# Kernel tuning notes

Hardware: AMD Instinct MI355X
Metric: run time of the kernel (lower is better)

Reference implementation:

```python
import jax, jax.numpy as jnp
import numpy as np

WIDE = 15
PAD = (WIDE - 1) // 2
FREQS = np.array([1., 2., 3., 4., 5., 6.], dtype=np.float32)  # wave_base_ml frequencies


def _lstm_dir(x, wih, whh, b):
    # x: [B,T,F]; wih: [4H,F]; whh: [4H,H]; b: [4H] (b_ih+b_hh fused)
    H = whh.shape[1]
    xg = jnp.einsum('btf,gf->btg', x, wih) + b  # precompute input projections
    def step(carry, xt):
        h, c = carry
        g = xt + h @ whh.T
        i, f, gg, o = jnp.split(g, 4, axis=-1)  # torch gate order i,f,g,o
        c = jax.nn.sigmoid(f) * c + jax.nn.sigmoid(i) * jnp.tanh(gg)
        h = jax.nn.sigmoid(o) * jnp.tanh(c)
        return (h, c), h
    h0 = jnp.zeros((x.shape[0], H), x.dtype)
    _, hs = jax.lax.scan(step, (h0, h0), jnp.swapaxes(xg, 0, 1))
    return jnp.swapaxes(hs, 0, 1)


def _bn(x, g, b, eps=1e-5):
    # training-mode BatchNorm1d over (N, L) per channel; x: [B,C,L]
    m = jnp.mean(x, axis=(0, 2), keepdims=True)
    v = jnp.var(x, axis=(0, 2), keepdims=True)
    return (x - m) * jax.lax.rsqrt(v + eps) * g[None, :, None] + b[None, :, None]


def _conv1d(x, w, b):
    y = jax.lax.conv_general_dilated(x, w, (1,), 'VALID', dimension_numbers=('NCH', 'OIH', 'NCH'))
    return y + b[None, :, None]


def _haar(x):
    s = 0.7071067811865476
    return (x[..., ::2] + x[..., 1::2]) * s, (x[..., ::2] - x[..., 1::2]) * s


def _forward(x, lstm_wif, lstm_whf, lstm_bf, lstm_wir, lstm_whr, lstm_br, base_w, base_b,
             g1, be1, g2, be2, g3, be3, g4, be4, g5, be5,
             w2, b2, w3, b3, w4, b4, w5, b5, fcw, fcb):
    xt = jnp.swapaxes(x, 1, 2)  # [B,T,F]
    fwd = _lstm_dir(xt, lstm_wif, lstm_whf, lstm_bf)
    bwd = _lstm_dir(xt[:, ::-1], lstm_wir, lstm_whr, lstm_br)[:, ::-1]
    X = jnp.swapaxes(jnp.concatenate([fwd, bwd], axis=-1), 1, 2)  # [B,C,T], C=2*dim
    B, C, T = X.shape
    Xp = jnp.pad(X, ((0, 0), (0, 0), (PAD, PAD)))
    # shared sliding windows [B,C,T,WIDE] used both for scale conv and Furi_conv
    Xwin = jnp.stack([Xp[..., k:k + T] for k in range(WIDE)], axis=-1)
    offs = (jnp.arange(WIDE, dtype=X.dtype) - PAD) / WIDE
    outs = []
    for ii in range(len(FREQS)):
        scales = jax.nn.relu(jnp.einsum('bctk,k->bct', Xwin, base_w[ii]) + base_b[ii])
        # per-position cosine Fourier basis generated from the learned scales
        bases = jnp.cos((2.0 * np.pi * FREQS[ii]) * scales[..., None] * offs)  # [B,C,T,WIDE]
        o = jnp.sum(Xwin * bases, axis=-1)  # position-dependent (dynamic) conv
        sqrs = jnp.sqrt((jnp.trunc(scales * WIDE) + 1.0) / (WIDE + 2) * 2.0)
        outs.append(o / sqrs)
    wave = jnp.stack(outs, axis=1).reshape(B, -1, T)  # [B, n_waves*C, T] (wave-major, matches torch cat+view)
    out = _bn(wave, g1, be1)
    out = _bn(jax.nn.relu(_conv1d(out, w2, b2)), g2, be2)
    out = _bn(jax.nn.relu(_conv1d(out, w3, b3)), g3, be3)
    out_back = out  # [B, V_dim, L3]
    out = _bn(jax.nn.relu(_conv1d(out, w4, b4)), g4, be4)  # [B,16,L3-2]
    # 4-level Haar DWT; 5 subbands upsampled to L3, averaged over channels
    a1, d1 = _haar(out_back); a2, d2 = _haar(a1); a3, d3 = _haar(a2); a4, d4 = _haar(a3)
    L3 = out_back.shape[-1]
    bands = [jnp.repeat(bb, L3 // bb.shape[-1], axis=-1) for bb in (a4, d4, d3, d2, d1)]
    dwt = jnp.stack([bb.mean(axis=1) for bb in bands], axis=1)  # [B,5,L3]
    odwt = _bn(jax.nn.relu(_conv1d(dwt, w5, b5)), g5, be5)  # [B,16,L3-2]
    out = jnp.concatenate([out, odwt], axis=-1)
    out = out.mean(axis=-1)  # AdaptiveAvgPool1d(1) + squeeze
    return out @ fcw.T + fcb


def setup_inputs() -> dict:
    key = jax.random.key(0)
    ks = iter(jax.random.split(key, 40))
    def p(shape, s=0.05):
        return jax.random.normal(next(ks), shape, jnp.float32) * s
    B, F, T, DIM, NW, Vd = 32, 64, 518, 64, 6, 32
    C = 2 * DIM
    return {
        'x': jax.random.normal(next(ks), (B, F, T), jnp.float32),
        'lstm_wif': p((4 * DIM, F)), 'lstm_whf': p((4 * DIM, DIM)), 'lstm_bf': p((4 * DIM,)),
        'lstm_wir': p((4 * DIM, F)), 'lstm_whr': p((4 * DIM, DIM)), 'lstm_br': p((4 * DIM,)),
        'base_w': p((NW, WIDE)), 'base_b': p((NW,)),
        'g1': jnp.ones((C * NW,)), 'be1': jnp.zeros((C * NW,)),
        'g2': jnp.ones((128,)), 'be2': jnp.zeros((128,)),
        'g3': jnp.ones((Vd,)), 'be3': jnp.zeros((Vd,)),
        'g4': jnp.ones((16,)), 'be4': jnp.zeros((16,)),
        'g5': jnp.ones((16,)), 'be5': jnp.zeros((16,)),
        'w2': p((128, C * NW, 3)), 'b2': p((128,)),
        'w3': p((Vd, 128, 5)), 'b3': p((Vd,)),
        'w4': p((16, Vd, 3)), 'b4': p((16,)),
        'w5': p((16, 5, 3)), 'b5': p((16,)),
        'fcw': p((10, 16)), 'fcb': p((10,)),
    }


def reference(x, lstm_wif, lstm_whf, lstm_bf, lstm_wir, lstm_whr, lstm_br, base_w, base_b,
              g1, be1, g2, be2, g3, be3, g4, be4, g5, be5,
              w2, b2, w3, b3, w4, b4, w5, b5, fcw, fcb):
    return _forward(x, lstm_wif, lstm_whf, lstm_bf, lstm_wir, lstm_whr, lstm_br, base_w, base_b,
                    g1, be1, g2, be2, g3, be3, g4, be4, g5, be5,
                    w2, b2, w3, b3, w4, b4, w5, b5, fcw, fcb)
```

## Files before the change

### kernel.cpp

```cpp
#include <hip/hip_runtime.h>
#include <math.h>

#define B_     32
#define F_     64
#define T_     518
#define HID    64
#define GATES  256
#define CCH    128
#define NWAVE  6
#define WCH    768
#define L2_    516
#define L3_    512
#define L4_    510

typedef float v2f __attribute__((ext_vector_type(2)));
typedef _Float16 h2 __attribute__((ext_vector_type(2)));

__device__ __forceinline__ float frcp(float x) { return __builtin_amdgcn_rcpf(x); }
__device__ __forceinline__ float fsigmoid(float x) { return frcp(1.f + __expf(-x)); }
__device__ __forceinline__ float ftanh(float x) { return 1.f - 2.f * frcp(1.f + __expf(2.f * x)); }

__device__ __forceinline__ float fdot2(h2 a, h2 b, float c) {
#if __has_builtin(__builtin_amdgcn_fdot2)
    return __builtin_amdgcn_fdot2(a, b, c, false);
#else
    return fmaf((float)a[0], (float)b[0], fmaf((float)a[1], (float)b[1], c));
#endif
}

__global__ void packw_kernel(const float* __restrict__ whf, const float* __restrict__ whr,
                             h2* __restrict__ w16f, h2* __restrict__ w16r) {
    const int row = threadIdx.x;
    const float* sf = whf + (size_t)row * HID;
    const float* sr = whr + (size_t)row * HID;
#pragma unroll
    for (int i = 0; i < 32; ++i) {
        w16f[row * 32 + i] = (h2){(_Float16)sf[2 * i], (_Float16)sf[2 * i + 1]};
        w16r[row * 32 + i] = (h2){(_Float16)sr[2 * i], (_Float16)sr[2 * i + 1]};
    }
}

__global__ void xg_kernel(const float* __restrict__ x,
                          const float* __restrict__ wif, const float* __restrict__ bf,
                          const float* __restrict__ wir, const float* __restrict__ br,
                          float* __restrict__ xg_f, float* __restrict__ xg_r,
                          float* __restrict__ stats, float* __restrict__ stats23) {
    if (blockIdx.x == 0 && blockIdx.y == 0) {
        for (int i = threadIdx.x; i < 2 * WCH; i += 256) stats[i] = 0.f;
        if (threadIdx.x < 320) stats23[threadIdx.x] = 0.f;
    }
    const int tid = threadIdx.x;
    const int wv  = tid >> 7;
    const int g2  = tid & 1;
    const int r   = (tid >> 1) & 63;
    const int g   = (2 * wv + g2) * 64 + r;
    const int b   = blockIdx.y;
    const int t0  = blockIdx.x * 8;
    float4 wa[16], wb[16];
    const float4* w0 = (const float4*)(wif + g * F_);
    const float4* w1 = (const float4*)(wir + g * F_);
#pragma unroll
    for (int i = 0; i < 16; ++i) { wa[i] = w0[i]; wb[i] = w1[i]; }
    const float bfv = bf[g], brv = br[g];
    for (int tt = 0; tt < 8; ++tt) {
        const int t = t0 + tt;
        if (t >= T_) break;
        const float* xp = x + (size_t)b * F_ * T_ + t;
        float a0 = bfv, a1 = brv;
#pragma unroll
        for (int i = 0; i < 16; ++i) {
            float x0 = xp[(i * 4 + 0) * T_];
            float x1 = xp[(i * 4 + 1) * T_];
            float x2 = xp[(i * 4 + 2) * T_];
            float x3 = xp[(i * 4 + 3) * T_];
            a0 += wa[i].x * x0 + wa[i].y * x1 + wa[i].z * x2 + wa[i].w * x3;
            a1 += wb[i].x * x0 + wb[i].y * x1 + wb[i].z * x2 + wb[i].w * x3;
        }
        const size_t o = ((size_t)b * T_ + t) * GATES + tid;
        xg_f[o] = a0;
        xg_r[o] = a1;
    }
}

__global__ __launch_bounds__(128, 1) void lstm_kernel(
        const float* __restrict__ xgi_f, const float* __restrict__ xgi_r,
        const h2* __restrict__ w16f, const h2* __restrict__ w16r,
        float* __restrict__ X) {
    const int dir = blockIdx.x & 1;
    const int b   = blockIdx.x >> 1;
    const float* xg  = (dir ? xgi_r : xgi_f) + (size_t)b * T_ * GATES;
    const h2* w16 = dir ? w16r : w16f;
    const int tid = threadIdx.x;
    const int r   = tid & 63;
    const int w   = tid >> 6;

    union U4 { uint4 u; h2 h[4]; };
    U4 wA[8], wB[8];
    {
        const uint4* pA = (const uint4*)(w16 + (size_t)((2 * w) * HID + r) * 32);
        const uint4* pB = (const uint4*)(w16 + (size_t)((2 * w + 1) * HID + r) * 32);
#pragma unroll
        for (int i = 0; i < 8; ++i) { wA[i].u = pA[i]; wB[i].u = pB[i]; }
    }

    __shared__ __align__(16) _Float16 hs16[2][HID];
    __shared__ __align__(16) float gbuf[2][HID][4];
    hs16[w][r] = (_Float16)0.f;
    float c = 0.f;
    float* Xrow = X + ((size_t)(b * CCH + dir * HID + r)) * T_;

    int t = dir ? (T_ - 1) : 0;
    const int step = dir ? -1 : 1;
    const float2* xg2 = (const float2*)xg;
    float2 q0 = xg2[((size_t)t * 2 + w) * 64 + r];
    float2 q1 = xg2[((size_t)(t + step) * 2 + w) * 64 + r];

    for (int s = 0; s < T_; ++s) {
        float a0 = q0.x, a0b = 0.f;
        float a1 = q0.y, a1b = 0.f;
        const uint4* hp4 = (const uint4*)hs16[w];
#pragma unroll
        for (int i = 0; i < 8; ++i) {
            U4 hv; hv.u = hp4[i];
            a0  = fdot2(wA[i].h[0], hv.h[0], a0);
            a0b = fdot2(wA[i].h[1], hv.h[1], a0b);
            a0  = fdot2(wA[i].h[2], hv.h[2], a0);
            a0b = fdot2(wA[i].h[3], hv.h[3], a0b);
            a1  = fdot2(wB[i].h[0], hv.h[0], a1);
            a1b = fdot2(wB[i].h[1], hv.h[1], a1b);
            a1  = fdot2(wB[i].h[2], hv.h[2], a1);
            a1b = fdot2(wB[i].h[3], hv.h[3], a1b);
        }
        const float gA = a0 + a0b;
        const float gB = a1 + a1b;
        const int buf = s & 1;
        *(float2*)&gbuf[buf][r][2 * w] = make_float2(gA, gB);

        int tp = t + 2 * step;
        tp = tp < 0 ? 0 : (tp >= T_ ? T_ - 1 : tp);
        const float2 qn = xg2[((size_t)tp * 2 + w) * 64 + r];

        asm volatile("s_waitcnt lgkmcnt(0)" ::: "memory");
        __builtin_amdgcn_s_barrier();

        const float4 g4 = *(const float4*)gbuf[buf][r];
        const float si = fsigmoid(g4.x);
        const float sf = fsigmoid(g4.y);
        const float so = fsigmoid(g4.w);
        c = sf * c + si * ftanh(g4.z);
        const float h = so * ftanh(c);

        hs16[w][r] = (_Float16)h;
        if (w == 0) Xrow[t] = h;
        q0 = q1; q1 = qn;
        t += step;
    }
}

__global__ void wave_kernel(const float* __restrict__ X,
                            const float* __restrict__ bw, const float* __restrict__ bb,
                            float* __restrict__ wave, float* __restrict__ stats) {
    const int b = blockIdx.z, c = blockIdx.y;
    const int t0 = blockIdx.x * 256;
    const int tid = threadIdx.x;
    __shared__ float xs[256 + 14];
    __shared__ float bws[NWAVE][16];
    __shared__ float bbs[NWAVE];
    __shared__ float red[4][12];
    const float* xrow = X + ((size_t)(b * CCH + c)) * T_;
    for (int i = tid; i < 270; i += 256) {
        int tt = t0 - 7 + i;
        xs[i] = (tt >= 0 && tt < T_) ? xrow[tt] : 0.f;
    }
    if (tid < NWAVE * 15) bws[tid / 15][tid % 15] = bw[tid];
    if (tid < NWAVE) bbs[tid] = bb[tid];
    __syncthreads();
    const int t = t0 + tid;
    float ls[NWAVE], lq[NWAVE];
#pragma unroll
    for (int ii = 0; ii < NWAVE; ++ii) { ls[ii] = 0.f; lq[ii] = 0.f; }
    if (t < T_) {
        float win[15];
#pragma unroll
        for (int k = 0; k < 15; ++k) win[k] = xs[tid + k];
        float e[8];
        e[0] = win[7];
#pragma unroll
        for (int m = 1; m < 8; ++m) e[m] = win[7 - m] + win[7 + m];
        const float c0 = 6.28318530717958647692f / 15.f;
#pragma unroll
        for (int ii = 0; ii < NWAVE; ++ii) {
            float sc = bbs[ii];
#pragma unroll
            for (int k = 0; k < 15; ++k) sc += win[k] * bws[ii][k];
            sc = fmaxf(sc, 0.f);
            const float phi = c0 * (float)(ii + 1) * sc;
            float o = e[0];
#pragma unroll
            for (int m = 1; m < 8; ++m) o += e[m] * __cosf(phi * (float)m);
            const float q = (truncf(sc * 15.f) + 1.f) * (2.f / 17.f);
            const float val = o * rsqrtf(q);
            wave[((size_t)(b * WCH + ii * CCH + c)) * T_ + t] = val;
            ls[ii] = val;
            lq[ii] = val * val;
        }
    }
#pragma unroll
    for (int off = 32; off > 0; off >>= 1) {
#pragma unroll
        for (int ii = 0; ii < NWAVE; ++ii) {
            ls[ii] += __shfl_down(ls[ii], off);
            lq[ii] += __shfl_down(lq[ii], off);
        }
    }
    if ((tid & 63) == 0) {
        const int w = tid >> 6;
#pragma unroll
        for (int ii = 0; ii < NWAVE; ++ii) { red[w][ii] = ls[ii]; red[w][6 + ii] = lq[ii]; }
    }
    __syncthreads();
    if (tid < 12) {
        const float a = red[0][tid] + red[1][tid] + red[2][tid] + red[3][tid];
        const int ii = tid % 6;
        const int ch = ii * CCH + c;
        atomicAdd(&stats[(tid >= 6 ? WCH : 0) + ch], a);
    }
}

__global__ void bn1_finalize_kernel(const float* __restrict__ stats,
                                    float* __restrict__ mean, float* __restrict__ rstd) {
    const int c = threadIdx.x;
    const float n = (float)(B_ * T_);
    const float m = stats[c] / n;
    const float v = stats[WCH + c] / n - m * m;
    mean[c] = m;
    rstd[c] = rsqrtf(v + 1e-5f);
}

__global__ void bnfold2_kernel(const float* __restrict__ w2, const float* __restrict__ b2,
                               const float* __restrict__ m1, const float* __restrict__ r1,
                               const float* __restrict__ g1, const float* __restrict__ be1,
                               float* __restrict__ w2t, float* __restrict__ b2t) {
    const int o = blockIdx.x, tid = threadIdx.x;
    float part = 0.f;
    for (int idx = tid; idx < WCH * 3; idx += 256) {
        const int c = idx / 3;
        const float sc = r1[c] * g1[c];
        const float sh = be1[c] - m1[c] * sc;
        const float wv = w2[(size_t)o * (WCH * 3) + idx];
        w2t[(size_t)idx * 128 + o] = wv * sc;
        part += wv * sh;
    }
#pragma unroll
    for (int off = 32; off > 0; off >>= 1) part += __shfl_down(part, off);
    __shared__ float red[4];
    if ((tid & 63) == 0) red[tid >> 6] = part;
    __syncthreads();
    if (tid == 0) b2t[o] = b2[o] + red[0] + red[1] + red[2] + red[3];
}

__global__ void bnfold3_kernel(const float* __restrict__ w3, const float* __restrict__ b3,
                               const float* __restrict__ stats2,
                               const float* __restrict__ g2, const float* __restrict__ be2,
                               float* __restrict__ w3t, float* __restrict__ b3t) {
    const int o = blockIdx.x, tid = threadIdx.x;
    __shared__ float sc2s[128], sh2s[128];
    if (tid < 128) {
        const float n = (float)(B_ * L2_);
        const float m = stats2[tid] / n;
        const float v = stats2[128 + tid] / n - m * m;
        const float sc = rsqrtf(v + 1e-5f) * g2[tid];
        sc2s[tid] = sc;
        sh2s[tid] = be2[tid] - m * sc;
    }
    __syncthreads();
    float part = 0.f;
    for (int idx = tid; idx < 128 * 5; idx += 256) {
        const int c = idx / 5;
        const float wv = w3[(size_t)o * 640 + idx];
        w3t[(size_t)idx * 32 + o] = wv * sc2s[c];
        part += wv * sh2s[c];
    }
#pragma unroll
    for (int off = 32; off > 0; off >>= 1) part += __shfl_down(part, off);
    __shared__ float red[4];
    if ((tid & 63) == 0) red[tid >> 6] = part;
    __syncthreads();
    if (tid == 0) b3t[o] = b3[o] + red[0] + red[1] + red[2] + red[3];
}

__global__ void bnfold4_kernel(const float* __restrict__ w4, const float* __restrict__ b4,
                               const float* __restrict__ stats3,
                               const float* __restrict__ g3, const float* __restrict__ be3,
                               float* __restrict__ w4t, float* __restrict__ b4t) {
    const int o = blockIdx.x, tid = threadIdx.x;
    __shared__ float sc3s[32], sh3s[32];
    if (tid < 32) {
        const float n = (float)(B_ * L3_);
        const float m = stats3[tid] / n;
        const float v = stats3[32 + tid] / n - m * m;
        const float sc = rsqrtf(v + 1e-5f) * g3[tid];
        sc3s[tid] = sc;
        sh3s[tid] = be3[tid] - m * sc;
    }
    __syncthreads();
    float part = 0.f;
    if (tid < 96) {
        const int c = tid / 3;
        const float wv = w4[(size_t)o * 96 + tid];
        w4t[(size_t)tid * 16 + o] = wv * sc3s[c];
        part = wv * sh3s[c];
    }
#pragma unroll
    for (int off = 32; off > 0; off >>= 1) part += __shfl_down(part, off);
    __shared__ float red[2];
    if ((tid & 63) == 0) red[tid >> 6] = part;
    __syncthreads();
    if (tid == 0) b4t[o] = b4[o] + red[0] + red[1];
}

__global__ __launch_bounds__(256) void conv2_kernel(
        const float* __restrict__ in, const float* __restrict__ wt,
        const float* __restrict__ bt, float* __restrict__ out,
        float* __restrict__ stats2) {
    const int b  = blockIdx.x;
    const int tid = threadIdx.x;
    const int t  = blockIdx.y * 256 + tid;
    const int o0 = blockIdx.z * 16;
    float rv[16], qv[16];
#pragma unroll
    for (int j = 0; j < 16; ++j) rv[j] = 0.f;
    if (t < L2_) {
        v2f acc[8];
        const v2f* bt2 = (const v2f*)(bt + o0);
#pragma unroll
        for (int j = 0; j < 8; ++j) acc[j] = bt2[j];
        const float* inb = in + (size_t)b * WCH * T_ + t;
        for (int c = 0; c < WCH; ++c) {
            const float x0 = inb[c * T_], x1 = inb[c * T_ + 1], x2 = inb[c * T_ + 2];
            const v2f vx0 = {x0, x0}, vx1 = {x1, x1}, vx2 = {x2, x2};
            const v2f* wc = (const v2f*)(wt + (size_t)c * 384 + o0);
#pragma unroll
            for (int j = 0; j < 8; ++j)
                acc[j] = __builtin_elementwise_fma(wc[j], vx0,
                         __builtin_elementwise_fma(wc[64 + j], vx1,
                         __builtin_elementwise_fma(wc[128 + j], vx2, acc[j])));
        }
        const size_t ob = ((size_t)b * 128 + o0) * L2_ + t;
#pragma unroll
        for (int j = 0; j < 8; ++j) {
            rv[2 * j]     = fmaxf(acc[j].x, 0.f);
            rv[2 * j + 1] = fmaxf(acc[j].y, 0.f);
            out[ob + (size_t)(2 * j) * L2_]     = rv[2 * j];
            out[ob + (size_t)(2 * j + 1) * L2_] = rv[2 * j + 1];
        }
    }
#pragma unroll
    for (int j = 0; j < 16; ++j) qv[j] = rv[j] * rv[j];
#pragma unroll
    for (int off = 32; off > 0; off >>= 1) {
#pragma unroll
        for (int j = 0; j < 16; ++j) {
            rv[j] += __shfl_down(rv[j], off);
            qv[j] += __shfl_down(qv[j], off);
        }
    }
    __shared__ float red2[4][32];
    if ((tid & 63) == 0) {
        const int wv = tid >> 6;
#pragma unroll
        for (int j = 0; j < 16; ++j) { red2[wv][j] = rv[j]; red2[wv][16 + j] = qv[j]; }
    }
    __syncthreads();
    if (tid < 32) {
        const float a = red2[0][tid] + red2[1][tid] + red2[2][tid] + red2[3][tid];
        atomicAdd(&stats2[(tid >= 16 ? 128 : 0) + o0 + (tid & 15)], a);
    }
}

__global__ __launch_bounds__(256) void conv3_kernel(
        const float* __restrict__ in, const float* __restrict__ wt,
        const float* __restrict__ bt, float* __restrict__ out,
        float* __restrict__ stats3) {
    const int b  = blockIdx.x;
    const int tid = threadIdx.x;
    const int t  = blockIdx.y * 256 + tid;
    const int o0 = blockIdx.z * 8;
    v2f acc[4];
    const v2f* bt2 = (const v2f*)(bt + o0);
#pragma unroll
    for (int j = 0; j < 4; ++j) acc[j] = bt2[j];
    const float* inb = in + (size_t)b * 128 * L2_ + t;
    for (int c = 0; c < 128; ++c) {
        const float x0 = inb[c * L2_], x1 = inb[c * L2_ + 1], x2 = inb[c * L2_ + 2];
        const float x3 = inb[c * L2_ + 3], x4 = inb[c * L2_ + 4];
        const v2f vx0 = {x0, x0}, vx1 = {x1, x1}, vx2 = {x2, x2}, vx3 = {x3, x3}, vx4 = {x4, x4};
        const v2f* wc = (const v2f*)(wt + (size_t)c * 160 + o0);
#pragma unroll
        for (int j = 0; j < 4; ++j)
            acc[j] = __builtin_elementwise_fma(wc[j], vx0,
                     __builtin_elementwise_fma(wc[16 + j], vx1,
                     __builtin_elementwise_fma(wc[32 + j], vx2,
                     __builtin_elementwise_fma(wc[48 + j], vx3,
                     __builtin_elementwise_fma(wc[64 + j], vx4, acc[j])))));
    }
    const size_t ob = ((size_t)b * 32 + o0) * L3_ + t;
    float rv[8], qv[8];
#pragma unroll
    for (int j = 0; j < 4; ++j) {
        rv[2 * j]     = fmaxf(acc[j].x, 0.f);
        rv[2 * j + 1] = fmaxf(acc[j].y, 0.f);
        out[ob + (size_t)(2 * j) * L3_]     = rv[2 * j];
        out[ob + (size_t)(2 * j + 1) * L3_] = rv[2 * j + 1];
    }
#pragma unroll
    for (int j = 0; j < 8; ++j) qv[j] = rv[j] * rv[j];
#pragma unroll
    for (int off = 32; off > 0; off >>= 1) {
#pragma unroll
        for (int j = 0; j < 8; ++j) {
            rv[j] += __shfl_down(rv[j], off);
            qv[j] += __shfl_down(qv[j], off);
        }
    }
    __shared__ float red3[4][16];
    if ((tid & 63) == 0) {
        const int wv = tid >> 6;
#pragma unroll
        for (int j = 0; j < 8; ++j) { red3[wv][j] = rv[j]; red3[wv][8 + j] = qv[j]; }
    }
    __syncthreads();
    if (tid < 16) {
        const float a = red3[0][tid] + red3[1][tid] + red3[2][tid] + red3[3][tid];
        atomicAdd(&stats3[(tid >= 8 ? 32 : 0) + o0 + (tid & 7)], a);
    }
}

__global__ __launch_bounds__(512) void tail_fused_kernel(
        const float* __restrict__ y3, const float* __restrict__ w4t,
        const float* __restrict__ b4t, const float* __restrict__ w5,
        const float* __restrict__ b5, const float* __restrict__ stats3,
        const float* __restrict__ g3, const float* __restrict__ be3,
        float* __restrict__ part) {
    const int b = blockIdx.x, l = threadIdx.x;
    __shared__ float cm[L3_];
    __shared__ float bands[5][L3_];
    __shared__ float w5s[240];
    __shared__ float b5s[16], b4s[16];
    __shared__ float sc3s[32], sh3s[32];
    __shared__ float redf[8][64];
    if (l < 240) w5s[l] = w5[l];
    if (l < 16) { b5s[l] = b5[l]; b4s[l] = b4t[l]; }
    if (l >= 256 && l < 288) {
        const int ch = l - 256;
        const float n = (float)(B_ * L3_);
        const float m = stats3[ch] / n;
        const float v = stats3[32 + ch] / n - m * m;
        const float sc = rsqrtf(v + 1e-5f) * g3[ch];
        sc3s[ch] = sc;
        sh3s[ch] = be3[ch] - m * sc;
    }
    __syncthreads();
    v2f a4[8];
    const v2f* b4s2 = (const v2f*)b4s;
#pragma unroll
    for (int j = 0; j < 8; ++j) a4[j] = (v2f){0.f, 0.f};
    const float* yb = y3 + (size_t)b * 32 * L3_ + l;
    if (l < L4_) {
#pragma unroll
        for (int j = 0; j < 8; ++j) a4[j] = b4s2[j];
        for (int c = 0; c < 32; ++c) {
            const float x0 = yb[c * L3_], x1 = yb[c * L3_ + 1], x2 = yb[c * L3_ + 2];
            const v2f vx0 = {x0, x0}, vx1 = {x1, x1}, vx2 = {x2, x2};
            const v2f* wc = (const v2f*)(w4t + (size_t)c * 48);
#pragma unroll
            for (int j = 0; j < 8; ++j)
                a4[j] = __builtin_elementwise_fma(wc[j], vx0,
                        __builtin_elementwise_fma(wc[8 + j], vx1,
                        __builtin_elementwise_fma(wc[16 + j], vx2, a4[j])));
        }
    }
    {
        float s = 0.f, shs = 0.f;
        for (int ch = 0; ch < 32; ++ch) {
            s = fmaf(yb[ch * L3_], sc3s[ch], s);
            shs += sh3s[ch];
        }
        cm[l] = (s + shs) * (1.f / 32.f);
    }
    __syncthreads();
    const float s1 = 0.70710678118654752440f;
    const float s2c = 0.5f;
    const float s3 = 0.35355339059327378f;
    const float s4 = 0.25f;
    const int b16 = l & ~15, b8 = l & ~7, b4v = l & ~3, b2v = l & ~1;
    float sa = 0.f, sb = 0.f;
#pragma unroll
    for (int i = 0; i < 8; ++i) { sa += cm[b16 + i]; sb += cm[b16 + 8 + i]; }
    bands[0][l] = (sa + sb) * s4;
    bands[1][l] = (sa - sb) * s4;
    float ta = 0.f, tb = 0.f;
#pragma unroll
    for (int i = 0; i < 4; ++i) { ta += cm[b8 + i]; tb += cm[b8 + 4 + i]; }
    bands[2][l] = (ta - tb) * s3;
    bands[3][l] = (cm[b4v] + cm[b4v + 1] - cm[b4v + 2] - cm[b4v + 3]) * s2c;
    bands[4][l] = (cm[b2v] - cm[b2v + 1]) * s1;
    __syncthreads();
    float s4v[16], q4v[16], s5v[16], q5v[16];
#pragma unroll
    for (int o = 0; o < 16; ++o) { s5v[o] = 0.f; }
    if (l < L4_) {
        float in3[5][3];
#pragma unroll
        for (int c = 0; c < 5; ++c) {
            in3[c][0] = bands[c][l]; in3[c][1] = bands[c][l + 1]; in3[c][2] = bands[c][l + 2];
        }
#pragma unroll
        for (int o = 0; o < 16; ++o) {
            float acc = b5s[o];
#pragma unroll
            for (int c = 0; c < 5; ++c) {
                const float* wp = &w5s[(o * 5 + c) * 3];
                acc += in3[c][0] * wp[0] + in3[c][1] * wp[1] + in3[c][2] * wp[2];
            }
            s5v[o] = fmaxf(acc, 0.f);
        }
    }
#pragma unroll
    for (int j = 0; j < 8; ++j) {
        const float v0 = (l < L4_) ? fmaxf(a4[j].x, 0.f) : 0.f;
        const float v1 = (l < L4_) ? fmaxf(a4[j].y, 0.f) : 0.f;
        s4v[2 * j] = v0; s4v[2 * j + 1] = v1;
        q4v[2 * j] = v0 * v0; q4v[2 * j + 1] = v1 * v1;
    }
#pragma unroll
    for (int o = 0; o < 16; ++o) q5v[o] = s5v[o] * s5v[o];
#pragma unroll
    for (int off = 32; off > 0; off >>= 1) {
#pragma unroll
        for (int o = 0; o < 16; ++o) {
            s4v[o] += __shfl_down(s4v[o], off);
            q4v[o] += __shfl_down(q4v[o], off);
            s5v[o] += __shfl_down(s5v[o], off);
            q5v[o] += __shfl_down(q5v[o], off);
        }
    }
    if ((l & 63) == 0) {
        const int wv = l >> 6;
#pragma unroll
        for (int o = 0; o < 16; ++o) {
            redf[wv][o]      = s4v[o];
            redf[wv][16 + o] = q4v[o];
            redf[wv][32 + o] = s5v[o];
            redf[wv][48 + o] = q5v[o];
        }
    }
    __syncthreads();
    if (l < 64) {
        float a = 0.f;
#pragma unroll
        for (int wv = 0; wv < 8; ++wv) a += redf[wv][l];
        part[(size_t)(b * 16 + (l & 15)) * 4 + (l >> 4)] = a;
    }
}

__global__ __launch_bounds__(512) void tail_final_kernel(
        const float* __restrict__ part,
        const float* __restrict__ g4, const float* __restrict__ be4,
        const float* __restrict__ g5, const float* __restrict__ be5,
        const float* __restrict__ fcw, const float* __restrict__ fcb,
        float* __restrict__ out) {
    const int p = threadIdx.x;
    const int b = p >> 4, ch = p & 15;
    const float4 v = ((const float4*)part)[b * 16 + ch];
    __shared__ float S4[512], Q4[512], S5[512], Q5[512];
    __shared__ float M4[16], R4[16], M5[16], R5[16];
    __shared__ float pool[B_][16];
    S4[p] = v.x; Q4[p] = v.y; S5[p] = v.z; Q5[p] = v.w;
    __syncthreads();
    if (p < 16) {
        float ts = 0.f, tq = 0.f, us = 0.f, uq = 0.f;
        for (int bb = 0; bb < B_; ++bb) {
            ts += S4[bb * 16 + p]; tq += Q4[bb * 16 + p];
            us += S5[bb * 16 + p]; uq += Q5[bb * 16 + p];
        }
        const float n = (float)(B_ * L4_);
        float m = ts / n; M4[p] = m; R4[p] = rsqrtf(tq / n - m * m + 1e-5f);
        m = us / n;       M5[p] = m; R5[p] = rsqrtf(uq / n - m * m + 1e-5f);
    }
    __syncthreads();
    {
        const float mm4 = v.x / (float)L4_, mm5 = v.z / (float)L4_;
        const float v4 = (mm4 - M4[ch]) * R4[ch] * g4[ch] + be4[ch];
        const float v5 = (mm5 - M5[ch]) * R5[ch] * g5[ch] + be5[ch];
        pool[b][ch] = 0.5f * (v4 + v5);
    }
    __syncthreads();
    if (p < B_ * 10) {
        const int bb = p / 10, row = p - bb * 10;
        float a = fcb[row];
#pragma unroll
        for (int c = 0; c < 16; ++c) a += pool[bb][c] * fcw[row * 16 + c];
        out[bb * 10 + row] = a;
    }
}

extern "C" void kernel_launch(void* const* d_in, const int* in_sizes, int n_in,
                              void* d_out, int out_size, void* d_ws, size_t ws_size,
                              hipStream_t stream) {
    (void)in_sizes; (void)n_in; (void)out_size; (void)ws_size;
    const float* x   = (const float*)d_in[0];
    const float* wif = (const float*)d_in[1];
    const float* whf = (const float*)d_in[2];
    const float* bf  = (const float*)d_in[3];
    const float* wir = (const float*)d_in[4];
    const float* whr = (const float*)d_in[5];
    const float* br  = (const float*)d_in[6];
    const float* bw  = (const float*)d_in[7];
    const float* bb  = (const float*)d_in[8];
    const float* g1  = (const float*)d_in[9];  const float* be1 = (const float*)d_in[10];
    const float* g2  = (const float*)d_in[11]; const float* be2 = (const float*)d_in[12];
    const float* g3  = (const float*)d_in[13]; const float* be3 = (const float*)d_in[14];
    const float* g4  = (const float*)d_in[15]; const float* be4 = (const float*)d_in[16];
    const float* g5  = (const float*)d_in[17]; const float* be5 = (const float*)d_in[18];
    const float* w2  = (const float*)d_in[19]; const float* b2  = (const float*)d_in[20];
    const float* w3  = (const float*)d_in[21]; const float* b3  = (const float*)d_in[22];
    const float* w4  = (const float*)d_in[23]; const float* b4  = (const float*)d_in[24];
    const float* w5  = (const float*)d_in[25]; const float* b5  = (const float*)d_in[26];
    const float* fcw = (const float*)d_in[27]; const float* fcb = (const float*)d_in[28];
    float* out = (float*)d_out;
    float* ws  = (float*)d_ws;

    float* xg_f  = ws;
    float* xg_r  = ws + 4243456;
    float* wave  = ws;
    float* X     = ws + 12730368;
    float* y2    = ws + 14852096;
    float* y3    = ws + 16965632;
    float* stats = ws + 18012160;
    float* m1 = ws + 18013696; float* r1 = m1 + 768;
    float* tpart  = r1 + 768;
    float* stats2 = tpart + 2048;
    float* stats3 = stats2 + 256;
    float* w2t  = X;
    float* b2t  = X + 294912;
    float* w3t  = X + 295040;
    float* b3t  = X + 315520;
    float* w4t  = X + 315552;
    float* b4t  = X + 317088;
    h2* w16f = (h2*)y2;
    h2* w16r = (h2*)(y2 + 8192);

    packw_kernel<<<dim3(1), 256, 0, stream>>>(whf, whr, w16f, w16r);
    xg_kernel<<<dim3(65, 32), 256, 0, stream>>>(x, wif, bf, wir, br, xg_f, xg_r,
                                                stats, stats2);
    lstm_kernel<<<dim3(64), 128, 0, stream>>>(xg_f, xg_r, w16f, w16r, X);
    wave_kernel<<<dim3(3, CCH, B_), 256, 0, stream>>>(X, bw, bb, wave, stats);
    bn1_finalize_kernel<<<dim3(1), 768, 0, stream>>>(stats, m1, r1);
    bnfold2_kernel<<<dim3(128), 256, 0, stream>>>(w2, b2, m1, r1, g1, be1, w2t, b2t);
    conv2_kernel<<<dim3(32, 3, 8), 256, 0, stream>>>(wave, w2t, b2t, y2, stats2);
    bnfold3_kernel<<<dim3(32), 256, 0, stream>>>(w3, b3, stats2, g2, be2, w3t, b3t);
    conv3_kernel<<<dim3(32, 2, 4), 256, 0, stream>>>(y2, w3t, b3t, y3, stats3);
    bnfold4_kernel<<<dim3(16), 128, 0, stream>>>(w4, b4, stats3, g3, be3, w4t, b4t);
    tail_fused_kernel<<<dim3(B_), 512, 0, stream>>>(y3, w4t, b4t, w5, b5,
                                                    stats3, g3, be3, tpart);
    tail_final_kernel<<<dim3(1), 512, 0, stream>>>(tpart, g4, be4, g5, be5, fcw, fcb, out);
}
```

Measured before the change: 881.5 us.

## Remove LSTM gate LDS exchange, split xg by direction, use cosine recurrence, widen conv2

The LSTM step now pairs gate halves across wave lanes with shfl_xor instead of staging them in shared memory, and double-buffers the hidden state so each step needs one barrier instead of a store/barrier/load round trip. The input-projection kernel launches a third grid dimension for direction, halving per-thread weight registers. The wave kernel computes cos(m*phi) with a Chebyshev recurrence instead of seven cosf calls, and conv2 computes 32 output channels per block instead of 16. Together these target the serial LSTM latency and the ALU cost elsewhere, at the price of more registers in conv2 and possible small numeric drift from the recurrence.

```diff
diff --git a/kernel.cpp b/kernel.cpp
--- a/kernel.cpp
+++ b/kernel.cpp
@@ -45,10 +45,14 @@
                           const float* __restrict__ wir, const float* __restrict__ br,
                           float* __restrict__ xg_f, float* __restrict__ xg_r,
                           float* __restrict__ stats, float* __restrict__ stats23) {
-    if (blockIdx.x == 0 && blockIdx.y == 0) {
+    if (blockIdx.x == 0 && blockIdx.y == 0 && blockIdx.z == 0) {
         for (int i = threadIdx.x; i < 2 * WCH; i += 256) stats[i] = 0.f;
         if (threadIdx.x < 320) stats23[threadIdx.x] = 0.f;
     }
+    const int dir = blockIdx.z;
+    const float* wi = dir ? wir : wif;
+    const float* bi = dir ? br : bf;
+    float* xgo = dir ? xg_r : xg_f;
     const int tid = threadIdx.x;
     const int wv  = tid >> 7;
     const int g2  = tid & 1;
@@ -56,17 +60,16 @@
     const int g   = (2 * wv + g2) * 64 + r;
     const int b   = blockIdx.y;
     const int t0  = blockIdx.x * 8;
-    float4 wa[16], wb[16];
-    const float4* w0 = (const float4*)(wif + g * F_);
-    const float4* w1 = (const float4*)(wir + g * F_);
-#pragma unroll
-    for (int i = 0; i < 16; ++i) { wa[i] = w0[i]; wb[i] = w1[i]; }
-    const float bfv = bf[g], brv = br[g];
+    float4 wa[16];
+    const float4* w0 = (const float4*)(wi + g * F_);
+#pragma unroll
+    for (int i = 0; i < 16; ++i) wa[i] = w0[i];
+    const float bv = bi[g];
     for (int tt = 0; tt < 8; ++tt) {
         const int t = t0 + tt;
         if (t >= T_) break;
         const float* xp = x + (size_t)b * F_ * T_ + t;
-        float a0 = bfv, a1 = brv;
+        float a0 = bv;
 #pragma unroll
         for (int i = 0; i < 16; ++i) {
             float x0 = xp[(i * 4 + 0) * T_];
@@ -74,11 +77,8 @@
             float x2 = xp[(i * 4 + 2) * T_];
             float x3 = xp[(i * 4 + 3) * T_];
             a0 += wa[i].x * x0 + wa[i].y * x1 + wa[i].z * x2 + wa[i].w * x3;
-            a1 += wb[i].x * x0 + wb[i].y * x1 + wb[i].z * x2 + wb[i].w * x3;
-        }
-        const size_t o = ((size_t)b * T_ + t) * GATES + tid;
-        xg_f[o] = a0;
-        xg_r[o] = a1;
+        }
+        xgo[((size_t)b * T_ + t) * GATES + tid] = a0;
     }
 }
 
@@ -91,37 +91,39 @@
     const float* xg  = (dir ? xgi_r : xgi_f) + (size_t)b * T_ * GATES;
     const h2* w16 = dir ? w16r : w16f;
     const int tid = threadIdx.x;
-    const int r   = tid & 63;
+    const int lw  = tid & 63;
     const int w   = tid >> 6;
-
-    union U4 { uint4 u; h2 h[4]; };
+    const int p   = lw >> 5;
+    const int u   = 32 * w + (lw & 31);
+
+    union U4 { uint4 u4; h2 h[4]; };
     U4 wA[8], wB[8];
     {
-        const uint4* pA = (const uint4*)(w16 + (size_t)((2 * w) * HID + r) * 32);
-        const uint4* pB = (const uint4*)(w16 + (size_t)((2 * w + 1) * HID + r) * 32);
-#pragma unroll
-        for (int i = 0; i < 8; ++i) { wA[i].u = pA[i]; wB[i].u = pB[i]; }
+        const uint4* pA = (const uint4*)(w16 + (size_t)((2 * p) * HID + u) * 32);
+        const uint4* pB = (const uint4*)(w16 + (size_t)((2 * p + 1) * HID + u) * 32);
+#pragma unroll
+        for (int i = 0; i < 8; ++i) { wA[i].u4 = pA[i]; wB[i].u4 = pB[i]; }
     }
 
     __shared__ __align__(16) _Float16 hs16[2][HID];
-    __shared__ __align__(16) float gbuf[2][HID][4];
-    hs16[w][r] = (_Float16)0.f;
+    if (lw < 32) { hs16[0][u] = (_Float16)0.f; hs16[1][u] = (_Float16)0.f; }
     float c = 0.f;
-    float* Xrow = X + ((size_t)(b * CCH + dir * HID + r)) * T_;
+    float* Xrow = X + ((size_t)(b * CCH + dir * HID + u)) * T_;
 
     int t = dir ? (T_ - 1) : 0;
     const int step = dir ? -1 : 1;
     const float2* xg2 = (const float2*)xg;
-    float2 q0 = xg2[((size_t)t * 2 + w) * 64 + r];
-    float2 q1 = xg2[((size_t)(t + step) * 2 + w) * 64 + r];
+    float2 q0 = xg2[((size_t)t * 2 + p) * 64 + u];
+    float2 q1 = xg2[((size_t)(t + step) * 2 + p) * 64 + u];
+    __syncthreads();
 
     for (int s = 0; s < T_; ++s) {
+        const uint4* hp4 = (const uint4*)hs16[(s + 1) & 1];
         float a0 = q0.x, a0b = 0.f;
         float a1 = q0.y, a1b = 0.f;
-        const uint4* hp4 = (const uint4*)hs16[w];
 #pragma unroll
         for (int i = 0; i < 8; ++i) {
-            U4 hv; hv.u = hp4[i];
+            U4 hv; hv.u4 = hp4[i];
             a0  = fdot2(wA[i].h[0], hv.h[0], a0);
             a0b = fdot2(wA[i].h[1], hv.h[1], a0b);
             a0  = fdot2(wA[i].h[2], hv.h[2], a0);
@@ -133,25 +135,27 @@
         }
         const float gA = a0 + a0b;
         const float gB = a1 + a1b;
-        const int buf = s & 1;
-        *(float2*)&gbuf[buf][r][2 * w] = make_float2(gA, gB);
+        const float oA = __shfl_xor(gA, 32, 64);
+        const float oB = __shfl_xor(gB, 32, 64);
+        const float gi = p ? oA : gA;
+        const float gf = p ? oB : gB;
+        const float gg = p ? gA : oA;
+        const float go = p ? gB : oB;
 
         int tp = t + 2 * step;
         tp = tp < 0 ? 0 : (tp >= T_ ? T_ - 1 : tp);
-        const float2 qn = xg2[((size_t)tp * 2 + w) * 64 + r];
-
+        const float2 qn = xg2[((size_t)tp * 2 + p) * 64 + u];
+
+        const float si = fsigmoid(gi);
+        const float sf = fsigmoid(gf);
+        const float so = fsigmoid(go);
+        c = sf * c + si * ftanh(gg);
+        const float h = so * ftanh(c);
+
+        if (lw < 32) { hs16[s & 1][u] = (_Float16)h; Xrow[t] = h; }
         asm volatile("s_waitcnt lgkmcnt(0)" ::: "memory");
         __builtin_amdgcn_s_barrier();
 
-        const float4 g4 = *(const float4*)gbuf[buf][r];
-        const float si = fsigmoid(g4.x);
-        const float sf = fsigmoid(g4.y);
-        const float so = fsigmoid(g4.w);
-        c = sf * c + si * ftanh(g4.z);
-        const float h = so * ftanh(c);
-
-        hs16[w][r] = (_Float16)h;
-        if (w == 0) Xrow[t] = h;
         q0 = q1; q1 = qn;
         t += step;
     }
@@ -195,9 +199,15 @@
             for (int k = 0; k < 15; ++k) sc += win[k] * bws[ii][k];
             sc = fmaxf(sc, 0.f);
             const float phi = c0 * (float)(ii + 1) * sc;
-            float o = e[0];
-#pragma unroll
-            for (int m = 1; m < 8; ++m) o += e[m] * __cosf(phi * (float)m);
+            const float c1 = __cosf(phi);
+            float o = fmaf(e[1], c1, e[0]);
+            float cp = 1.f, cc = c1;
+#pragma unroll
+            for (int m = 2; m < 8; ++m) {
+                const float cn = fmaf(2.f * c1, cc, -cp);
+                o = fmaf(e[m], cn, o);
+                cp = cc; cc = cn;
+            }
             const float q = (truncf(sc * 15.f) + 1.f) * (2.f / 17.f);
             const float val = o * rsqrtf(q);
             wave[((size_t)(b * WCH + ii * CCH + c)) * T_ + t] = val;
@@ -326,29 +336,29 @@
     const int b  = blockIdx.x;
     const int tid = threadIdx.x;
     const int t  = blockIdx.y * 256 + tid;
-    const int o0 = blockIdx.z * 16;
-    float rv[16], qv[16];
-#pragma unroll
-    for (int j = 0; j < 16; ++j) rv[j] = 0.f;
+    const int o0 = blockIdx.z * 32;
+    float rv[32], qv[32];
+#pragma unroll
+    for (int j = 0; j < 32; ++j) rv[j] = 0.f;
     if (t < L2_) {
-        v2f acc[8];
+        v2f acc[16];
         const v2f* bt2 = (const v2f*)(bt + o0);
 #pragma unroll
-        for (int j = 0; j < 8; ++j) acc[j] = bt2[j];
+        for (int j = 0; j < 16; ++j) acc[j] = bt2[j];
         const float* inb = in + (size_t)b * WCH * T_ + t;
         for (int c = 0; c < WCH; ++c) {
             const float x0 = inb[c * T_], x1 = inb[c * T_ + 1], x2 = inb[c * T_ + 2];
             const v2f vx0 = {x0, x0}, vx1 = {x1, x1}, vx2 = {x2, x2};
             const v2f* wc = (const v2f*)(wt + (size_t)c * 384 + o0);
 #pragma unroll
-            for (int j = 0; j < 8; ++j)
+            for (int j = 0; j < 16; ++j)
                 acc[j] = __builtin_elementwise_fma(wc[j], vx0,
                          __builtin_elementwise_fma(wc[64 + j], vx1,
                          __builtin_elementwise_fma(wc[128 + j], vx2, acc[j])));
         }
         const size_t ob = ((size_t)b * 128 + o0) * L2_ + t;
 #pragma unroll
-        for (int j = 0; j < 8; ++j) {
+        for (int j = 0; j < 16; ++j) {
             rv[2 * j]     = fmaxf(acc[j].x, 0.f);
             rv[2 * j + 1] = fmaxf(acc[j].y, 0.f);
             out[ob + (size_t)(2 * j) * L2_]     = rv[2 * j];
@@ -356,25 +366,25 @@
         }
     }
 #pragma unroll
-    for (int j = 0; j < 16; ++j) qv[j] = rv[j] * rv[j];
+    for (int j = 0; j < 32; ++j) qv[j] = rv[j] * rv[j];
 #pragma unroll
     for (int off = 32; off > 0; off >>= 1) {
 #pragma unroll
-        for (int j = 0; j < 16; ++j) {
+        for (int j = 0; j < 32; ++j) {
             rv[j] += __shfl_down(rv[j], off);
             qv[j] += __shfl_down(qv[j], off);
         }
     }
-    __shared__ float red2[4][32];
+    __shared__ float red2[4][64];
     if ((tid & 63) == 0) {
         const int wv = tid >> 6;
 #pragma unroll
-        for (int j = 0; j < 16; ++j) { red2[wv][j] = rv[j]; red2[wv][16 + j] = qv[j]; }
-    }
-    __syncthreads();
-    if (tid < 32) {
+        for (int j = 0; j < 32; ++j) { red2[wv][j] = rv[j]; red2[wv][32 + j] = qv[j]; }
+    }
+    __syncthreads();
+    if (tid < 64) {
         const float a = red2[0][tid] + red2[1][tid] + red2[2][tid] + red2[3][tid];
-        atomicAdd(&stats2[(tid >= 16 ? 128 : 0) + o0 + (tid & 15)], a);
+        atomicAdd(&stats2[(tid >= 32 ? 128 : 0) + o0 + (tid & 31)], a);
     }
 }
 
@@ -652,13 +662,13 @@
     h2* w16r = (h2*)(y2 + 8192);
 
     packw_kernel<<<dim3(1), 256, 0, stream>>>(whf, whr, w16f, w16r);
-    xg_kernel<<<dim3(65, 32), 256, 0, stream>>>(x, wif, bf, wir, br, xg_f, xg_r,
-                                                stats, stats2);
+    xg_kernel<<<dim3(65, 32, 2), 256, 0, stream>>>(x, wif, bf, wir, br, xg_f, xg_r,
+                                                   stats, stats2);
     lstm_kernel<<<dim3(64), 128, 0, stream>>>(xg_f, xg_r, w16f, w16r, X);
     wave_kernel<<<dim3(3, CCH, B_), 256, 0, stream>>>(X, bw, bb, wave, stats);
     bn1_finalize_kernel<<<dim3(1), 768, 0, stream>>>(stats, m1, r1);
     bnfold2_kernel<<<dim3(128), 256, 0, stream>>>(w2, b2, m1, r1, g1, be1, w2t, b2t);
-    conv2_kernel<<<dim3(32, 3, 8), 256, 0, stream>>>(wave, w2t, b2t, y2, stats2);
+    conv2_kernel<<<dim3(32, 3, 4), 256, 0, stream>>>(wave, w2t, b2t, y2, stats2);
     bnfold3_kernel<<<dim3(32), 256, 0, stream>>>(w3, b3, stats2, g2, be2, w3t, b3t);
     conv3_kernel<<<dim3(32, 2, 4), 256, 0, stream>>>(y2, w3t, b3t, y3, stats3);
     bnfold4_kernel<<<dim3(16), 128, 0, stream>>>(w4, b4, stats3, g3, be3, w4t, b4t);
```

New measurement: 1.051 ms. 19.3% more time.
